# Kernel optimization log

Measured on AMD Instinct MI355X. Metric: run time of the kernel, lower is better.

Reference implementation:

```python
import jax, jax.numpy as jnp
import numpy as np

DIM = 1024
DIM_FEAT = 384
HIDDEN = 1024
HEADS = 16
D_HEAD = HIDDEN // HEADS
SCALE = D_HEAD ** -0.5
EPS = 1e-5


def _layernorm(x, g, b):
    mu = jnp.mean(x, axis=-1, keepdims=True)
    var = jnp.var(x, axis=-1, keepdims=True)
    return (x - mu) * jax.lax.rsqrt(var + EPS) * g + b


def _split_heads(t):
    b, n, _ = t.shape
    return t.reshape(b, n, HEADS, D_HEAD).transpose(0, 2, 1, 3)  # b h n d


def _merge_heads(t):
    b, h, n, d = t.shape
    return t.transpose(0, 2, 1, 3).reshape(b, n, h * d)


def _attn(q, k, v):
    dots = jnp.einsum('bhnd,bhmd->bhnm', q, k) * SCALE
    attn = jax.nn.softmax(dots, axis=-1)
    return jnp.einsum('bhnm,bhmd->bhnd', attn, v)


def setup_inputs() -> dict:
    key = jax.random.key(0)
    ks = jax.random.split(key, 10)
    B, N = 2, 2048
    s = lambda fan: 1.0 / np.sqrt(fan)
    return {
        'x': jax.random.normal(ks[0], (B, N, DIM), jnp.float32),
        'feature': jax.random.normal(ks[1], (B, N, DIM_FEAT), jnp.float32),
        'norm_g': jnp.ones((DIM,), jnp.float32),
        'norm_b': jnp.zeros((DIM,), jnp.float32),
        'W_cq': jax.random.normal(ks[2], (DIM, HIDDEN), jnp.float32) * s(DIM),
        'W_ckv': jax.random.normal(ks[3], (DIM_FEAT, 2 * HIDDEN), jnp.float32) * s(DIM_FEAT),
        'W_sqkv': jax.random.normal(ks[4], (DIM, 3 * HIDDEN), jnp.float32) * s(DIM),
        'ffn_g': jnp.ones((DIM,), jnp.float32),
        'ffn_b': jnp.zeros((DIM,), jnp.float32),
        'W1': jax.random.normal(ks[5], (DIM, 4 * DIM), jnp.float32) * s(DIM),
        'b1': jnp.zeros((4 * DIM,), jnp.float32),
        'W2': jax.random.normal(ks[6], (4 * DIM, DIM), jnp.float32) * s(4 * DIM),
        'b2': jnp.zeros((DIM,), jnp.float32),
    }


def reference(x, feature, norm_g, norm_b, W_cq, W_ckv, W_sqkv, ffn_g, ffn_b, W1, b1, W2, b2):
    # cross attention
    xn = _layernorm(x, norm_g, norm_b)
    q = _split_heads(xn @ W_cq)
    kv = feature @ W_ckv
    k, v = jnp.split(kv, 2, axis=-1)
    cross = _merge_heads(_attn(q, _split_heads(k), _split_heads(v))) + x
    # self attention (shared norm)
    cn = _layernorm(cross, norm_g, norm_b)
    qkv = cn @ W_sqkv
    sq, sk, sv = (_split_heads(t) for t in jnp.split(qkv, 3, axis=-1))
    self_tok = _merge_heads(_attn(sq, sk, sv)) + cross
    # FFN with its own layernorm
    h = _layernorm(self_tok, ffn_g, ffn_b)
    h = jax.nn.gelu(h @ W1 + b1, approximate=False)
    out = h @ W2 + b2
    return out + self_tok
```

## Files before the change

kernel.cpp:

```cpp
#include <hip/hip_runtime.h>
#include <math.h>
#include <stdint.h>

typedef __attribute__((ext_vector_type(8)))  short   short8;
typedef __attribute__((ext_vector_type(4)))  short   short4v;
typedef __attribute__((ext_vector_type(8)))  __bf16  bf16x8;
typedef __attribute__((ext_vector_type(4)))  float   f32x4;
typedef __attribute__((ext_vector_type(16))) float   f32x16;

__device__ __forceinline__ unsigned short f2b(float f) {
    union { float f; unsigned u; } v; v.f = f;
    unsigned r = v.u + 0x7FFF + ((v.u >> 16) & 1);
    return (unsigned short)(r >> 16);
}

__device__ __forceinline__ f32x4 mfma_bf16(bf16x8 a, bf16x8 b, f32x4 c) {
    return __builtin_amdgcn_mfma_f32_16x16x32_bf16(a, b, c, 0, 0, 0);
}

__device__ __forceinline__ f32x16 mfma32(bf16x8 a, bf16x8 b, f32x16 c) {
    return __builtin_amdgcn_mfma_f32_32x32x16_bf16(a, b, c, 0, 0, 0);
}

__device__ __forceinline__ unsigned cvt_pk_bf16(float lo, float hi) {
    unsigned r;
    asm volatile("v_cvt_pk_bf16_f32 %0, %1, %2" : "=v"(r) : "v"(lo), "v"(hi));
    return r;
}

__device__ __forceinline__ void gload_lds16(const unsigned short* g, unsigned short* l) {
    __builtin_amdgcn_global_load_lds(
        (const __attribute__((address_space(1))) void*)g,
        (__attribute__((address_space(3))) void*)l,
        16, 0, 0);
}

template <int N>
__device__ __forceinline__ void wait_vmcnt() {
    if constexpr (N == 0)       asm volatile("s_waitcnt vmcnt(0)" ::: "memory");
    else if constexpr (N == 6)  asm volatile("s_waitcnt vmcnt(6)" ::: "memory");
    else if constexpr (N == 8)  asm volatile("s_waitcnt vmcnt(8)" ::: "memory");
    else                        static_assert(N == 0 || N == 6 || N == 8, "add vmcnt case");
}

#define QSCALE 0.18033688011112042592f

__global__ __launch_bounds__(256) void wconv_t(const float* __restrict__ W,
                                               unsigned short* __restrict__ Wt,
                                               int K, int N) {
    __shared__ float tile[32][33];
    int bk = blockIdx.x * 32;
    int bn = blockIdx.y * 32;
    int tx = threadIdx.x & 31, ty = threadIdx.x >> 5;
#pragma unroll
    for (int i = 0; i < 4; ++i) {
        int r = ty + i * 8;
        tile[r][tx] = W[(size_t)(bk + r) * N + bn + tx];
    }
    __syncthreads();
#pragma unroll
    for (int i = 0; i < 4; ++i) {
        int r = ty + i * 8;
        Wt[(size_t)(bn + r) * K + bk + tx] = f2b(tile[tx][r]);
    }
}

__global__ __launch_bounds__(256) void fconv(const float* __restrict__ in,
                                             unsigned short* __restrict__ out, int n4) {
    int i = blockIdx.x * 256 + threadIdx.x;
    if (i >= n4) return;
    f32x4 v = ((const f32x4*)in)[i];
    short4v o;
    o.x = (short)f2b(v.x); o.y = (short)f2b(v.y);
    o.z = (short)f2b(v.z); o.w = (short)f2b(v.w);
    ((short4v*)out)[i] = o;
}

__global__ __launch_bounds__(256) void lnorm(const float* __restrict__ x,
                                             const float* __restrict__ g,
                                             const float* __restrict__ bta,
                                             unsigned short* __restrict__ out) {
    int row = blockIdx.x;
    const f32x4* xr = (const f32x4*)(x + (size_t)row * 1024);
    int t = threadIdx.x;
    f32x4 v = xr[t];
    float s  = v.x + v.y + v.z + v.w;
    float s2 = v.x * v.x + v.y * v.y + v.z * v.z + v.w * v.w;
#pragma unroll
    for (int m = 1; m < 64; m <<= 1) {
        s  += __shfl_xor(s, m);
        s2 += __shfl_xor(s2, m);
    }
    __shared__ float rs[8];
    int w = t >> 6;
    if ((t & 63) == 0) { rs[w] = s; rs[4 + w] = s2; }
    __syncthreads();
    s  = rs[0] + rs[1] + rs[2] + rs[3];
    s2 = rs[4] + rs[5] + rs[6] + rs[7];
    float mean = s * (1.0f / 1024.0f);
    float var  = s2 * (1.0f / 1024.0f) - mean * mean;
    float rstd = rsqrtf(var + 1e-5f);
    f32x4 gv = ((const f32x4*)g)[t];
    f32x4 bv = ((const f32x4*)bta)[t];
    short4v o;
    o.x = (short)f2b((v.x - mean) * rstd * gv.x + bv.x);
    o.y = (short)f2b((v.y - mean) * rstd * gv.y + bv.y);
    o.z = (short)f2b((v.z - mean) * rstd * gv.z + bv.z);
    o.w = (short)f2b((v.w - mean) * rstd * gv.w + bv.w);
    ((short4v*)(out + (size_t)row * 1024))[t] = o;
}

template <int WM, int WN, int MI, int NI, int EPI, bool SCQ>
__global__ __launch_bounds__(WM * WN * 64, 2)
void gemm8(const unsigned short* __restrict__ A,
           const unsigned short* __restrict__ Bt,
           void* __restrict__ C,
           const float* __restrict__ bias,
           const float* __restrict__ resid,
           int M, int N, int K, int scale_cols) {
    constexpr int BM = WM * MI * 16;
    constexpr int BN = WN * NI * 16;
    constexpr int THREADS = WM * WN * 64;
    constexpr int ROWS = THREADS / 8;
    constexpr int IA = BM / ROWS;
    constexpr int IB = BN / ROWS;

    const int nwg = gridDim.x;
    const int nby = N / BN;
    int flat = blockIdx.x;
    int wk = (flat & 7) * (nwg >> 3) + (flat >> 3);
    const int m0 = (wk / nby) * BM;
    const int n0 = (wk % nby) * BN;

    __shared__ unsigned short As[2][BM * 64];
    __shared__ unsigned short Bs[2][BN * 64];

    const int tid  = threadIdx.x;
    const int lane = tid & 63;
    const int wid  = tid >> 6;
    const int wm = wid / WN, wn = wid % WN;
    const int l15 = lane & 15, q4 = lane >> 4, xw = lane & 7;

    const int sr = tid >> 3;
    const int sg = (tid & 7) ^ (sr & 7);

    const unsigned short* ag = A  + (size_t)(m0 + sr) * K + sg * 8;
    const unsigned short* bg = Bt + (size_t)(n0 + sr) * K + sg * 8;

    f32x4 acc[MI][NI] = {};

    auto STAGE = [&](int d, int t) {
        const int k0 = t * 64;
#pragma unroll
        for (int i = 0; i < IA; ++i)
            gload_lds16(ag + (size_t)(i * ROWS) * K + k0, &As[d][i * ROWS * 64 + tid * 8]);
#pragma unroll
        for (int i = 0; i < IB; ++i)
            gload_lds16(bg + (size_t)(i * ROWS) * K + k0, &Bs[d][i * ROWS * 64 + tid * 8]);
    };

    const int NT = K >> 6;
    STAGE(0, 0);

    for (int t = 0; t < NT; ++t) {
        const int c = t & 1;
        if (t + 1 < NT) STAGE(c ^ 1, t + 1);
        __builtin_amdgcn_sched_barrier(0);
        if (t + 1 < NT) wait_vmcnt<IA + IB>();
        else            wait_vmcnt<0>();
        __builtin_amdgcn_s_barrier();
        __builtin_amdgcn_sched_barrier(0);
#pragma unroll
        for (int h = 0; h < 2; ++h) {
            bf16x8 a[MI], b[NI];
            const int gsl = h * 4 + q4;
#pragma unroll
            for (int mi = 0; mi < MI; ++mi)
                a[mi] = *(const bf16x8*)&As[c][(wm * MI * 16 + mi * 16 + l15) * 64 + ((gsl ^ xw) << 3)];
#pragma unroll
            for (int ni = 0; ni < NI; ++ni)
                b[ni] = *(const bf16x8*)&Bs[c][(wn * NI * 16 + ni * 16 + l15) * 64 + ((gsl ^ xw) << 3)];
            __builtin_amdgcn_s_setprio(1);
#pragma unroll
            for (int mi = 0; mi < MI; ++mi)
#pragma unroll
                for (int ni = 0; ni < NI; ++ni)
                    acc[mi][ni] = mfma_bf16(a[mi], b[ni], acc[mi][ni]);
            __builtin_amdgcn_s_setprio(0);
        }
        __builtin_amdgcn_sched_barrier(0);
        __builtin_amdgcn_s_barrier();
    }

    const int rb = m0 + wm * MI * 16 + q4 * 4;
    const int cb = n0 + wn * NI * 16 + l15;
    float bv[NI];
    if (EPI >= 1) {
#pragma unroll
        for (int ni = 0; ni < NI; ++ni) bv[ni] = bias[cb + ni * 16];
    }
#pragma unroll
    for (int mi = 0; mi < MI; ++mi) {
#pragma unroll
        for (int r = 0; r < 4; ++r) {
            const int row = rb + mi * 16 + r;
#pragma unroll
            for (int ni = 0; ni < NI; ++ni) {
                const int col = cb + ni * 16;
                float v = acc[mi][ni][r];
                if (EPI == 0) {
                    if (SCQ && col < scale_cols) v *= QSCALE;
                    ((unsigned short*)C)[(size_t)row * N + col] = f2b(v);
                } else if (EPI == 1) {
                    v += bv[ni];
                    v = 0.5f * v * (1.0f + erff(v * 0.70710678118f));
                    ((unsigned short*)C)[(size_t)row * N + col] = f2b(v);
                } else {
                    v += bv[ni] + resid[(size_t)row * N + col];
                    ((float*)C)[(size_t)row * N + col] = v;
                }
            }
        }
    }
}

__global__ __launch_bounds__(256) void vtrans(const unsigned short* __restrict__ src,
                                              unsigned short* __restrict__ dst,
                                              int src_stride, int col_off) {
    int n0 = blockIdx.x * 64;
    int bh = blockIdx.y;
    int b = bh >> 4, h = bh & 15;
    __shared__ unsigned short t[64][65];
    int tx = threadIdx.x & 63, ty = threadIdx.x >> 6;
    const unsigned short* s = src + (size_t)(b * 2048 + n0) * src_stride + col_off + h * 64;
#pragma unroll
    for (int i = 0; i < 16; ++i) {
        int n = ty * 16 + i;
        t[n][tx] = s[(size_t)n * src_stride + tx];
    }
    __syncthreads();
    unsigned short* d = dst + (size_t)bh * 64 * 2048 + n0;
#pragma unroll
    for (int i = 0; i < 16; ++i) {
        int dd = ty * 16 + i;
        d[(size_t)dd * 2048 + tx] = t[tx][dd];
    }
}

__global__ __launch_bounds__(256) void attn(const unsigned short* __restrict__ Q, int q_stride, int q_off,
                                            const unsigned short* __restrict__ Kp, int k_stride, int k_off,
                                            const unsigned short* __restrict__ Vt,
                                            const float* __restrict__ res,
                                            float* __restrict__ out) {
    const int bid = blockIdx.x;
    const int slot = bid >> 3;
    const int bh = (bid & 7) * 4 + (slot >> 4);
    const int qt = slot & 15;
    const int b = bh >> 4, h = bh & 15;
    const int lane = threadIdx.x & 63, w = threadIdx.x >> 6;
    const int l31 = lane & 31, l5 = lane >> 5;

    __shared__ unsigned short Ks[2][64 * 64];
    __shared__ unsigned short Vs[2][64 * 64];

    const int q0 = qt * 128 + w * 32;

    const unsigned short* qp = Q + (size_t)(b * 2048 + q0 + l31) * q_stride + q_off + h * 64 + l5 * 8;
    bf16x8 qf[4];
#pragma unroll
    for (int i = 0; i < 4; ++i) qf[i] = *(const bf16x8*)&qp[i * 16];

    const unsigned short* kg = Kp + (size_t)(b * 2048) * k_stride + k_off + h * 64;
    const unsigned short* vg = Vt + (size_t)bh * 64 * 2048;

    const int sgrow = lane >> 3;
    const int sgcol = (((lane & 7) ^ sgrow) << 3);

    f32x16 oacc[2] = {};
    float m = -1e30f, l = 0.f;

    const int kxor = (l31 & 7) << 3;

#pragma unroll
    for (int t8 = 0; t8 < 2; ++t8) {
        const int rb = w * 16 + t8 * 8;
        gload_lds16(kg + (size_t)(rb + sgrow) * k_stride + sgcol, &Ks[0][rb * 64]);
        gload_lds16(vg + (size_t)(rb + sgrow) * 2048 + sgcol,     &Vs[0][rb * 64]);
    }
    __syncthreads();

    for (int t = 0; t < 32; ++t) {
        const int cur = t & 1;
        if (t + 1 < 32) {
            const int n1 = (t + 1) * 64;
#pragma unroll
            for (int t8 = 0; t8 < 2; ++t8) {
                const int rb = w * 16 + t8 * 8;
                gload_lds16(kg + (size_t)(n1 + rb + sgrow) * k_stride + sgcol, &Ks[cur ^ 1][rb * 64]);
                gload_lds16(vg + (size_t)(rb + sgrow) * 2048 + n1 + sgcol,     &Vs[cur ^ 1][rb * 64]);
            }
        }

        bf16x8 kf[2][4];
#pragma unroll
        for (int ks = 0; ks < 2; ++ks)
#pragma unroll
            for (int i = 0; i < 4; ++i)
                kf[ks][i] = *(const bf16x8*)&Ks[cur][(ks * 32 + l31) * 64 + ((i * 16 + l5 * 8) ^ kxor)];

        f32x16 s0 = {}, s1 = {};
#pragma unroll
        for (int i = 0; i < 4; ++i) s0 = mfma32(kf[0][i], qf[i], s0);
#pragma unroll
        for (int i = 0; i < 4; ++i) s1 = mfma32(kf[1][i], qf[i], s1);

        bf16x8 vf[2][4];
#pragma unroll
        for (int dh = 0; dh < 2; ++dh)
#pragma unroll
            for (int c = 0; c < 4; ++c)
                vf[dh][c] = *(const bf16x8*)&Vs[cur][(dh * 32 + l31) * 64 + ((c * 16 + l5 * 8) ^ kxor)];

        float mx = s0[0];
#pragma unroll
        for (int r = 1; r < 16; ++r) mx = fmaxf(mx, s0[r]);
#pragma unroll
        for (int r = 0; r < 16; ++r) mx = fmaxf(mx, s1[r]);
        mx = fmaxf(mx, __shfl_xor(mx, 32));
        if (!__all(mx - m <= 8.f)) {
            float mnew = fmaxf(m, mx);
            float al = __builtin_amdgcn_exp2f(m - mnew);
            m = mnew;
            l *= al;
#pragma unroll
            for (int dh = 0; dh < 2; ++dh)
#pragma unroll
                for (int r = 0; r < 16; ++r) oacc[dh][r] *= al;
        }
        float p0[16], p1[16];
        float ssum = 0.f;
#pragma unroll
        for (int r = 0; r < 16; ++r) { p0[r] = __builtin_amdgcn_exp2f(s0[r] - m); ssum += p0[r]; }
#pragma unroll
        for (int r = 0; r < 16; ++r) { p1[r] = __builtin_amdgcn_exp2f(s1[r] - m); ssum += p1[r]; }
        ssum += __shfl_xor(ssum, 32);
        l += ssum;

        bf16x8 pf[4];
#pragma unroll
        for (int half = 0; half < 2; ++half) {
            const float* p = half ? p1 : p0;
#pragma unroll
            for (int c = 0; c < 2; ++c) {
                unsigned a0 = cvt_pk_bf16(p[8 * c + 0], p[8 * c + 1]);
                unsigned a1 = cvt_pk_bf16(p[8 * c + 4], p[8 * c + 5]);
                unsigned b0 = cvt_pk_bf16(p[8 * c + 2], p[8 * c + 3]);
                unsigned b1 = cvt_pk_bf16(p[8 * c + 6], p[8 * c + 7]);
                asm volatile("v_permlane32_swap_b32 %0, %1" : "+v"(a0), "+v"(a1));
                asm volatile("v_permlane32_swap_b32 %0, %1" : "+v"(b0), "+v"(b1));
                union { unsigned u[4]; bf16x8 v; } pu;
                pu.u[0] = a0; pu.u[1] = b0; pu.u[2] = a1; pu.u[3] = b1;
                pf[half * 2 + c] = pu.v;
            }
        }

#pragma unroll
        for (int dh = 0; dh < 2; ++dh)
#pragma unroll
            for (int c = 0; c < 4; ++c)
                oacc[dh] = mfma32(vf[dh][c], pf[c], oacc[dh]);

        __syncthreads();
    }

    const float inv = 1.0f / l;
    const size_t rowoff = (size_t)(b * 2048 + q0 + l31) * 1024 + h * 64;
#pragma unroll
    for (int dh = 0; dh < 2; ++dh) {
#pragma unroll
        for (int g = 0; g < 4; ++g) {
            const int col = dh * 32 + g * 8 + l5 * 4;
            f32x4 rv = *(const f32x4*)&res[rowoff + col];
            f32x4 ov;
#pragma unroll
            for (int r = 0; r < 4; ++r) ov[r] = oacc[dh][g * 4 + r] * inv + rv[r];
            *(f32x4*)&out[rowoff + col] = ov;
        }
    }
}

extern "C" void kernel_launch(void* const* d_in, const int* in_sizes, int n_in,
                              void* d_out, int out_size, void* d_ws, size_t ws_size,
                              hipStream_t stream) {
    const float* x      = (const float*)d_in[0];
    const float* feat   = (const float*)d_in[1];
    const float* norm_g = (const float*)d_in[2];
    const float* norm_b = (const float*)d_in[3];
    const float* W_cq   = (const float*)d_in[4];
    const float* W_ckv  = (const float*)d_in[5];
    const float* W_sqkv = (const float*)d_in[6];
    const float* ffn_g  = (const float*)d_in[7];
    const float* ffn_b  = (const float*)d_in[8];
    const float* W1     = (const float*)d_in[9];
    const float* b1     = (const float*)d_in[10];
    const float* W2     = (const float*)d_in[11];
    const float* b2     = (const float*)d_in[12];
    float* out = (float*)d_out;

    char* ws = (char*)d_ws;
    unsigned short* wq_t   = (unsigned short*)(ws + (size_t)(0u)   * (1u << 20));
    unsigned short* wkv_t  = (unsigned short*)(ws + (size_t)(2u)   * (1u << 20));
    unsigned short* wqkv_t = (unsigned short*)(ws + (size_t)(4u)   * (1u << 20));
    unsigned short* w1_t   = (unsigned short*)(ws + (size_t)(10u)  * (1u << 20));
    unsigned short* w2_t   = (unsigned short*)(ws + (size_t)(18u)  * (1u << 20));
    unsigned short* featb  = (unsigned short*)(ws + (size_t)(26u)  * (1u << 20));
    unsigned short* t0     = (unsigned short*)(ws + (size_t)(29u)  * (1u << 20));
    float*          cross  = (float*)        (ws + (size_t)(37u)  * (1u << 20));
    unsigned short* qb     = (unsigned short*)(ws + (size_t)(53u)  * (1u << 20));
    unsigned short* kvb    = (unsigned short*)(ws + (size_t)(61u)  * (1u << 20));
    unsigned short* qkvb   = (unsigned short*)(ws + (size_t)(77u)  * (1u << 20));
    unsigned short* vtb    = (unsigned short*)(ws + (size_t)(101u) * (1u << 20));
    unsigned short* h1     = (unsigned short*)(ws + (size_t)(53u)  * (1u << 20));

    wconv_t<<<dim3(1024 / 32, 1024 / 32), 256, 0, stream>>>(W_cq,   wq_t,   1024, 1024);
    wconv_t<<<dim3(384 / 32,  2048 / 32), 256, 0, stream>>>(W_ckv,  wkv_t,  384,  2048);
    wconv_t<<<dim3(1024 / 32, 3072 / 32), 256, 0, stream>>>(W_sqkv, wqkv_t, 1024, 3072);
    wconv_t<<<dim3(1024 / 32, 4096 / 32), 256, 0, stream>>>(W1,     w1_t,   1024, 4096);
    wconv_t<<<dim3(4096 / 32, 1024 / 32), 256, 0, stream>>>(W2,     w2_t,   4096, 1024);
    fconv<<<dim3((4096 * 384 / 4) / 256), 256, 0, stream>>>(feat, featb, 4096 * 384 / 4);

    lnorm<<<4096, 256, 0, stream>>>(x, norm_g, norm_b, t0);
    gemm8<2, 2, 4, 2, 0, true ><<<512, 256, 0, stream>>>(t0,    wq_t,  qb,  nullptr, nullptr, 4096, 1024, 1024, 1024);
    gemm8<2, 2, 4, 4, 0, false><<<512, 256, 0, stream>>>(featb, wkv_t, kvb, nullptr, nullptr, 4096, 2048, 384,  0);
    vtrans<<<dim3(32, 32), 256, 0, stream>>>(kvb, vtb, 2048, 1024);
    attn<<<512, 256, 0, stream>>>(qb, 1024, 0, kvb, 2048, 0, vtb, x, cross);

    lnorm<<<4096, 256, 0, stream>>>(cross, norm_g, norm_b, t0);
    gemm8<2, 2, 4, 2, 0, true ><<<1536, 256, 0, stream>>>(t0, wqkv_t, qkvb, nullptr, nullptr, 4096, 3072, 1024, 1024);
    vtrans<<<dim3(32, 32), 256, 0, stream>>>(qkvb, vtb, 3072, 2048);
    attn<<<512, 256, 0, stream>>>(qkvb, 3072, 0, qkvb, 3072, 1024, vtb, cross, out);

    lnorm<<<4096, 256, 0, stream>>>(out, ffn_g, ffn_b, t0);
    gemm8<2, 2, 4, 4, 1, false><<<1024, 256, 0, stream>>>(t0, w1_t, h1, b1, nullptr, 4096, 4096, 1024, 0);
    gemm8<2, 2, 4, 2, 2, false><<<512, 256, 0, stream>>>(h1, w2_t, out, b2, (const float*)out, 4096, 1024, 4096, 0);
}
```

Measured before the change: 349.3 us.

## Restructure attention kernel: 2-wave blocks, new LDS layout, vmcnt pipelining, setprio

The attention kernel now uses 128-thread blocks covering 64 query rows, doubling the grid to 1024 blocks. K/V tiles are staged into a single LDS buffer with a column-group layout that replaces the XOR swizzle. Synchronisation changes from __syncthreads to explicit vmcnt waits plus s_barrier so the next tile's loads stay in flight. MFMA sections run at raised priority, and the row max and row sum use tree reductions instead of serial chains. Smaller blocks mean each K/V tile is loaded by more blocks, so global and L2 traffic goes up, and the new LDS layout may introduce bank conflicts.

Result: slower. 384.8 us (+10.2%).

```diff
diff --git a/kernel.cpp b/kernel.cpp
--- a/kernel.cpp
+++ b/kernel.cpp
@@ -247,23 +247,22 @@
     }
 }
 
-__global__ __launch_bounds__(256) void attn(const unsigned short* __restrict__ Q, int q_stride, int q_off,
+__global__ __launch_bounds__(128) void attn(const unsigned short* __restrict__ Q, int q_stride, int q_off,
                                             const unsigned short* __restrict__ Kp, int k_stride, int k_off,
                                             const unsigned short* __restrict__ Vt,
                                             const float* __restrict__ res,
                                             float* __restrict__ out) {
     const int bid = blockIdx.x;
     const int slot = bid >> 3;
-    const int bh = (bid & 7) * 4 + (slot >> 4);
-    const int qt = slot & 15;
+    const int bh = (bid & 7) * 4 + (slot >> 5);
+    const int qt = slot & 31;
     const int b = bh >> 4, h = bh & 15;
     const int lane = threadIdx.x & 63, w = threadIdx.x >> 6;
     const int l31 = lane & 31, l5 = lane >> 5;
 
-    __shared__ unsigned short Ks[2][64 * 64];
-    __shared__ unsigned short Vs[2][64 * 64];
-
-    const int q0 = qt * 128 + w * 32;
+    __shared__ unsigned short lds[2][8192];
+
+    const int q0 = qt * 64 + w * 32;
 
     const unsigned short* qp = Q + (size_t)(b * 2048 + q0 + l31) * q_stride + q_off + h * 64 + l5 * 8;
     bf16x8 qf[4];
@@ -273,60 +272,65 @@
     const unsigned short* kg = Kp + (size_t)(b * 2048) * k_stride + k_off + h * 64;
     const unsigned short* vg = Vt + (size_t)bh * 64 * 2048;
 
-    const int sgrow = lane >> 3;
-    const int sgcol = (((lane & 7) ^ sgrow) << 3);
-
     f32x16 oacc[2] = {};
     float m = -1e30f, l = 0.f;
 
-    const int kxor = (l31 & 7) << 3;
-
-#pragma unroll
-    for (int t8 = 0; t8 < 2; ++t8) {
-        const int rb = w * 16 + t8 * 8;
-        gload_lds16(kg + (size_t)(rb + sgrow) * k_stride + sgcol, &Ks[0][rb * 64]);
-        gload_lds16(vg + (size_t)(rb + sgrow) * 2048 + sgcol,     &Vs[0][rb * 64]);
-    }
-    __syncthreads();
+    auto STAGE = [&](int d, int t) {
+        const int n0 = t * 64;
+#pragma unroll
+        for (int j = 0; j < 4; ++j) {
+            const int g = w * 4 + j;
+            gload_lds16(kg + (size_t)(n0 + lane) * k_stride + g * 8, &lds[d][g * 512]);
+            gload_lds16(vg + (size_t)lane * 2048 + n0 + g * 8,       &lds[d][4096 + g * 512]);
+        }
+    };
+
+    STAGE(0, 0);
+    asm volatile("s_waitcnt vmcnt(0)" ::: "memory");
+    __builtin_amdgcn_s_barrier();
 
     for (int t = 0; t < 32; ++t) {
         const int cur = t & 1;
-        if (t + 1 < 32) {
-            const int n1 = (t + 1) * 64;
-#pragma unroll
-            for (int t8 = 0; t8 < 2; ++t8) {
-                const int rb = w * 16 + t8 * 8;
-                gload_lds16(kg + (size_t)(n1 + rb + sgrow) * k_stride + sgcol, &Ks[cur ^ 1][rb * 64]);
-                gload_lds16(vg + (size_t)(rb + sgrow) * 2048 + n1 + sgcol,     &Vs[cur ^ 1][rb * 64]);
-            }
-        }
+        if (t + 1 < 32) STAGE(cur ^ 1, t + 1);
+        __builtin_amdgcn_sched_barrier(0);
+        if (t + 1 < 32) wait_vmcnt<8>();
+        else            wait_vmcnt<0>();
+        __builtin_amdgcn_s_barrier();
+        __builtin_amdgcn_sched_barrier(0);
+
+        const unsigned short* Kc = &lds[cur][0];
+        const unsigned short* Vc = &lds[cur][4096];
 
         bf16x8 kf[2][4];
 #pragma unroll
         for (int ks = 0; ks < 2; ++ks)
 #pragma unroll
             for (int i = 0; i < 4; ++i)
-                kf[ks][i] = *(const bf16x8*)&Ks[cur][(ks * 32 + l31) * 64 + ((i * 16 + l5 * 8) ^ kxor)];
+                kf[ks][i] = *(const bf16x8*)&Kc[(i * 2 + l5) * 512 + ks * 256 + l31 * 8];
 
         f32x16 s0 = {}, s1 = {};
+        __builtin_amdgcn_s_setprio(1);
 #pragma unroll
         for (int i = 0; i < 4; ++i) s0 = mfma32(kf[0][i], qf[i], s0);
 #pragma unroll
         for (int i = 0; i < 4; ++i) s1 = mfma32(kf[1][i], qf[i], s1);
+        __builtin_amdgcn_s_setprio(0);
 
         bf16x8 vf[2][4];
 #pragma unroll
         for (int dh = 0; dh < 2; ++dh)
 #pragma unroll
             for (int c = 0; c < 4; ++c)
-                vf[dh][c] = *(const bf16x8*)&Vs[cur][(dh * 32 + l31) * 64 + ((c * 16 + l5 * 8) ^ kxor)];
-
-        float mx = s0[0];
-#pragma unroll
-        for (int r = 1; r < 16; ++r) mx = fmaxf(mx, s0[r]);
-#pragma unroll
-        for (int r = 0; r < 16; ++r) mx = fmaxf(mx, s1[r]);
-        mx = fmaxf(mx, __shfl_xor(mx, 32));
+                vf[dh][c] = *(const bf16x8*)&Vc[(c * 2 + l5) * 512 + dh * 256 + l31 * 8];
+
+        float tr[16];
+#pragma unroll
+        for (int r = 0; r < 16; ++r) tr[r] = fmaxf(s0[r], s1[r]);
+#pragma unroll
+        for (int off = 8; off >= 1; off >>= 1)
+#pragma unroll
+            for (int r = 0; r < off; ++r) tr[r] = fmaxf(tr[r], tr[r + off]);
+        float mx = fmaxf(tr[0], __shfl_xor(tr[0], 32));
         if (!__all(mx - m <= 8.f)) {
             float mnew = fmaxf(m, mx);
             float al = __builtin_amdgcn_exp2f(m - mnew);
@@ -338,13 +342,18 @@
                 for (int r = 0; r < 16; ++r) oacc[dh][r] *= al;
         }
         float p0[16], p1[16];
-        float ssum = 0.f;
-#pragma unroll
-        for (int r = 0; r < 16; ++r) { p0[r] = __builtin_amdgcn_exp2f(s0[r] - m); ssum += p0[r]; }
-#pragma unroll
-        for (int r = 0; r < 16; ++r) { p1[r] = __builtin_amdgcn_exp2f(s1[r] - m); ssum += p1[r]; }
-        ssum += __shfl_xor(ssum, 32);
-        l += ssum;
+#pragma unroll
+        for (int r = 0; r < 16; ++r) p0[r] = __builtin_amdgcn_exp2f(s0[r] - m);
+#pragma unroll
+        for (int r = 0; r < 16; ++r) p1[r] = __builtin_amdgcn_exp2f(s1[r] - m);
+        float sm[16];
+#pragma unroll
+        for (int r = 0; r < 16; ++r) sm[r] = p0[r] + p1[r];
+#pragma unroll
+        for (int off = 8; off >= 1; off >>= 1)
+#pragma unroll
+            for (int r = 0; r < off; ++r) sm[r] += sm[r + off];
+        l += sm[0] + __shfl_xor(sm[0], 32);
 
         bf16x8 pf[4];
 #pragma unroll
@@ -364,13 +373,15 @@
             }
         }
 
+        __builtin_amdgcn_s_setprio(1);
 #pragma unroll
         for (int dh = 0; dh < 2; ++dh)
 #pragma unroll
             for (int c = 0; c < 4; ++c)
                 oacc[dh] = mfma32(vf[dh][c], pf[c], oacc[dh]);
-
-        __syncthreads();
+        __builtin_amdgcn_s_setprio(0);
+
+        __builtin_amdgcn_s_barrier();
     }
 
     const float inv = 1.0f / l;
@@ -433,12 +444,12 @@
     gemm8<2, 2, 4, 2, 0, true ><<<512, 256, 0, stream>>>(t0,    wq_t,  qb,  nullptr, nullptr, 4096, 1024, 1024, 1024);
     gemm8<2, 2, 4, 4, 0, false><<<512, 256, 0, stream>>>(featb, wkv_t, kvb, nullptr, nullptr, 4096, 2048, 384,  0);
     vtrans<<<dim3(32, 32), 256, 0, stream>>>(kvb, vtb, 2048, 1024);
-    attn<<<512, 256, 0, stream>>>(qb, 1024, 0, kvb, 2048, 0, vtb, x, cross);
+    attn<<<1024, 128, 0, stream>>>(qb, 1024, 0, kvb, 2048, 0, vtb, x, cross);
 
     lnorm<<<4096, 256, 0, stream>>>(cross, norm_g, norm_b, t0);
     gemm8<2, 2, 4, 2, 0, true ><<<1536, 256, 0, stream>>>(t0, wqkv_t, qkvb, nullptr, nullptr, 4096, 3072, 1024, 1024);
     vtrans<<<dim3(32, 32), 256, 0, stream>>>(qkvb, vtb, 3072, 2048);
-    attn<<<512, 256, 0, stream>>>(qkvb, 3072, 0, qkvb, 3072, 1024, vtb, cross, out);
+    attn<<<1024, 128, 0, stream>>>(qkvb, 3072, 0, qkvb, 3072, 1024, vtb, cross, out);
 
     lnorm<<<4096, 256, 0, stream>>>(out, ffn_g, ffn_b, t0);
     gemm8<2, 2, 4, 4, 1, false><<<1024, 256, 0, stream>>>(t0, w1_t, h1, b1, nullptr, 4096, 4096, 1024, 0);
```
